# Kernel optimization log

Hardware: AMD Instinct MI355X
Metric: run time of the kernel (lower is better)

## Reference

```python
import jax, jax.numpy as jnp
import numpy as np

B, N, M, DN, DE, WN, WE, P = 16, 128, 1024, 512, 256, 128, 128, 512
EMB = WN + WE            # nenn embedding size per node / per edge
CLS_IN = 2 * EMB // 1    # = 2*wn + 2*we = 512
LR_OUT, CR_OUT, MR_OUT = 9, 6, 17
HID = 256


def _mk_params(key):
    ks = jax.random.split(key, 16)
    s = 0.02
    p = {
        'Wn':  jax.random.normal(ks[0], (DN, WN), jnp.float32) * s,
        'We':  jax.random.normal(ks[1], (DE, WE), jnp.float32) * s,
        'Wn2': jax.random.normal(ks[2], (DN, WN), jnp.float32) * s,
        'We2': jax.random.normal(ks[3], (DE, WE), jnp.float32) * s,
    }
    for i, h in enumerate(['scr', 'lr', 'mr']):
        out = {'scr': CR_OUT, 'lr': LR_OUT, 'mr': MR_OUT}[h]
        p[h + '_W1'] = jax.random.normal(ks[4 + 4 * i], (2 * EMB, HID), jnp.float32) * s
        p[h + '_b1'] = jnp.zeros((HID,), jnp.float32)
        p[h + '_W2'] = jax.random.normal(ks[5 + 4 * i], (HID, out), jnp.float32) * s
        p[h + '_b2'] = jnp.zeros((out,), jnp.float32)
    return p


def setup_inputs() -> dict:
    key = jax.random.key(0)
    ks = jax.random.split(key, 10)
    inp = {
        'node_features': jax.random.normal(ks[0], (B, N, DN), jnp.float32),
        'edge_features': jax.random.normal(ks[1], (B, N, N, DE), jnp.float32),
        'adj_mat': (jax.random.uniform(ks[2], (B, N, N)) < 0.1).astype(jnp.float32),
        'line_adj_mat': (jax.random.uniform(ks[3], (B, M, M)) < 0.02).astype(jnp.float32),
        'edge_index': jax.random.randint(ks[4], (B, 2, M), 0, N, jnp.int32),
        'object_pairs': jax.random.randint(ks[5], (B, P, 2), 0, N, jnp.int32),
        'num_obj': jax.random.randint(ks[6], (B,), N // 4, N + 1, jnp.int32),
        'num_edges': jax.random.randint(ks[7], (B,), M // 4, M + 1, jnp.int32),
    }
    inp.update(_mk_params(ks[8]))
    return inp


def _mlp(x, W1, b1, W2, b2):
    return jax.nn.relu(x @ W1 + b1) @ W2 + b2


def _forward(node_features, edge_features, adj_mat, line_adj_mat,
             Wn, We, Wn2, We2,
             scr_W1, scr_b1, scr_W2, scr_b2,
             lr_W1, lr_b1, lr_W2, lr_b2,
             mr_W1, mr_b1, mr_W2, mr_b2,
             edge_index, object_pairs, num_obj, num_edges):
    dt = node_features.dtype
    # ragged slicing [:num_obj] / [:num_edges] expressed as masks (padding stays 0)
    nmask = (jnp.arange(N) < num_obj[:, None]).astype(dt)      # [B,N]
    emask = (jnp.arange(M) < num_edges[:, None]).astype(dt)    # [B,M]

    X = node_features * nmask[..., None]                        # [B,N,DN]
    A = (adj_mat * nmask[:, :, None] * nmask[:, None, :]
         + jnp.eye(N, dtype=dt)[None] * nmask[:, :, None])      # A + I, masked
    h = jax.nn.relu((A @ X) @ Wn) * nmask[..., None]            # [B,N,WN] node-level emb

    src, dst = edge_index[:, 0], edge_index[:, 1]               # [B,M]
    Eg = jax.vmap(lambda e, s, d: e[s, d])(edge_features, src, dst)  # [B,M,DE]
    Eg = Eg * emask[..., None]
    L = (line_adj_mat * emask[:, :, None] * emask[:, None, :]
         + jnp.eye(M, dtype=dt)[None] * emask[:, :, None])      # line graph A + I
    g = jax.nn.relu((L @ Eg) @ We) * emask[..., None]           # [B,M,WE] edge-level emb

    # aggregate edge embeddings onto their source nodes (ragged scatter-add)
    agg = jax.vmap(lambda gb, sb: jnp.zeros((N, WE), gb.dtype).at[sb].add(gb))(g, src)
    node_emb = jnp.concatenate([h, agg * nmask[..., None]], -1)  # [B,N,EMB]

    # dense pairwise edge embeddings [B,N,N,EMB]
    Xp = X @ Wn2                                                 # [B,N,WN]
    Pm = jax.nn.relu(Xp[:, :, None, :] + Xp[:, None, :, :])      # node part [B,N,N,WN]
    Q = jax.nn.relu(edge_features @ We2)                         # edge part [B,N,N,WE]
    edge_emb = jnp.concatenate([Pm, Q], -1)

    # make_classifier_inputs: fused ragged gather instead of python double loop
    p0, p1 = object_pairs[..., 0], object_pairs[..., 1]          # [B,P]
    emb0 = jnp.take_along_axis(node_emb, p0[:, :, None], axis=1)  # [B,P,EMB]
    emb1 = jnp.take_along_axis(node_emb, p1[:, :, None], axis=1)
    eedge = jax.vmap(lambda eb, a, b: eb[a, b])(edge_emb, p0, p1)  # [B,P,EMB]
    ci = jnp.concatenate([emb0 + emb1, eedge], -1)               # aggregator='sum'

    lr = _mlp(ci, lr_W1, lr_b1, lr_W2, lr_b2)
    cr = _mlp(ci, scr_W1, scr_b1, scr_W2, scr_b2)
    mr = _mlp(ci, mr_W1, mr_b1, mr_W2, mr_b2)
    return lr, cr, mr


def reference(node_features, edge_features, adj_mat, line_adj_mat,
              edge_index, object_pairs, num_obj, num_edges,
              Wn, We, Wn2, We2,
              scr_W1, scr_b1, scr_W2, scr_b2,
              lr_W1, lr_b1, lr_W2, lr_b2,
              mr_W1, mr_b1, mr_W2, mr_b2):
    return _forward(node_features, edge_features, adj_mat, line_adj_mat,
                    Wn, We, Wn2, We2,
                    scr_W1, scr_b1, scr_W2, scr_b2,
                    lr_W1, lr_b1, lr_W2, lr_b2,
                    mr_W1, mr_b1, mr_W2, mr_b2,
                    edge_index, object_pairs, num_obj, num_edges)
```

## Files before the change

kernel.cpp:

```cpp
#include <hip/hip_runtime.h>
#include <hip/hip_bf16.h>
#include <cstdint>
#include <cstddef>

#define BB 16
#define NN 128
#define MM 1024
#define DN 512
#define DE 256
#define WN 128
#define WE 128
#define PP 512
#define HIDW 256
#define CIW 512

typedef __attribute__((ext_vector_type(8))) short s16x8;
typedef __attribute__((ext_vector_type(4))) float f32x4;

__device__ __forceinline__ float bf2f(unsigned short u) {
    unsigned int x = ((unsigned int)u) << 16;
    union { unsigned int i; float f; } c; c.i = x; return c.f;
}
__device__ __forceinline__ short f2b(float f) {
    __hip_bfloat16 h = __float2bfloat16(f);
    return *reinterpret_cast<short*>(&h);
}

__device__ __forceinline__ void gl_lds16(const ushort* g, ushort* l) {
    __builtin_amdgcn_global_load_lds(
        (const __attribute__((address_space(1))) unsigned int*)g,
        (__attribute__((address_space(3))) unsigned int*)l,
        16, 0, 0);
}

__global__ __launch_bounds__(256) void k0_prep(
    const float* __restrict__ lrW1, const float* __restrict__ scrW1,
    const float* __restrict__ mrW1,
    const float* __restrict__ lrb1, const float* __restrict__ scrb1,
    const float* __restrict__ mrb1,
    const float* __restrict__ Wn, const float* __restrict__ Wn2,
    const float* __restrict__ We, const float* __restrict__ We2,
    __hip_bfloat16* __restrict__ W1t, __hip_bfloat16* __restrict__ WncT,
    __hip_bfloat16* __restrict__ WeT, __hip_bfloat16* __restrict__ We2T,
    float* __restrict__ b1cat)
{
    int blk = blockIdx.x;
    int t = threadIdx.x;
    if (blk < 768) {
        int h = blk >> 8, n = blk & 255;
        const float* W = (h == 0) ? lrW1 : (h == 1) ? scrW1 : mrW1;
        W1t[(size_t)blk * 512 + t]       = __float2bfloat16(W[t * 256 + n]);
        W1t[(size_t)blk * 512 + t + 256] = __float2bfloat16(W[(t + 256) * 256 + n]);
    } else if (blk == 768) {
        b1cat[t]       = lrb1[t];
        b1cat[256 + t] = scrb1[t];
        b1cat[512 + t] = mrb1[t];
    } else if (blk < 897) {
        int n = blk - 769;
        WeT[(size_t)n * 256 + t] = __float2bfloat16(We[t * 128 + n]);
    } else if (blk < 1153) {
        int n = blk - 897;
        const float* W = (n < 128) ? Wn : Wn2;
        int c = n & 127;
        WncT[(size_t)n * 512 + t]       = __float2bfloat16(W[t * 128 + c]);
        WncT[(size_t)n * 512 + t + 256] = __float2bfloat16(W[(t + 256) * 128 + c]);
    } else {
        int n = blk - 1153;
        We2T[(size_t)n * 256 + t] = __float2bfloat16(We2[t * 128 + n]);
    }
}

__global__ __launch_bounds__(256) void fproj(
    const float* __restrict__ nf, const float* __restrict__ ef,
    const int* __restrict__ eidx, const int* __restrict__ opair,
    const int* __restrict__ nobj, const int* __restrict__ nedg,
    const ushort* __restrict__ WncT, const ushort* __restrict__ WeT,
    const ushort* __restrict__ We2T,
    float* __restrict__ Y, float* __restrict__ Xp,
    float* __restrict__ G1, __hip_bfloat16* __restrict__ ci)
{
    __shared__ ushort As[128 * 32];
    __shared__ ushort Bs[128 * 32];
    __shared__ unsigned rowoff[128];
    __shared__ float    rowval[128];

    int blk = blockIdx.x;
    int route, mb, nb, K;
    const ushort* Bt;
    if (blk < 32)       { route = 0; mb = blk >> 1;  nb = blk & 1; K = 512; Bt = WncT; }
    else if (blk < 160) { route = 1; mb = blk - 32;  nb = 0;       K = 256; Bt = WeT;  }
    else                { route = 2; mb = blk - 160; nb = 0;       K = 256; Bt = We2T; }
    int row0 = mb * 128, col0 = nb * 128;
    int t = threadIdx.x;

    if (t < 128) {
        int r = row0 + t;
        unsigned off; float valid = 1.f;
        if (route == 0) {
            int b = r >> 7, i = r & 127;
            off = (unsigned)r * DN;
            valid = (i < nobj[b]) ? 1.f : 0.f;
        } else if (route == 1) {
            int b = r >> 10, m = r & 1023;
            int src = eidx[b * 2 * MM + m];
            int dst = eidx[b * 2 * MM + MM + m];
            off = (unsigned)((b * NN + src) * NN + dst) * DE;
            valid = (m < nedg[b]) ? 1.f : 0.f;
        } else {
            int r2 = r;
            int b = r2 >> 9, p = r2 & 511;
            int i0 = opair[(b * PP + p) * 2];
            int i1 = opair[(b * PP + p) * 2 + 1];
            off = (unsigned)((b * NN + i0) * NN + i1) * DE;
        }
        rowoff[t] = off; rowval[t] = valid;
    }

    const float* Asrc = (route == 0) ? nf : ef;
    int lane = t & 63;
    int w    = t >> 6;
    int wr   = w >> 1, wc = w & 1;
    int arow = w * 32 + (lane >> 2);
    int ak   = (lane & 3) * 8;
    int qk   = (lane >> 4) * 8;
    int fr   = lane & 15;
    int sr   = t >> 2;
    int sk   = (t & 3) * 8;
    f32x4 acc[4][4];
    #pragma unroll
    for (int i = 0; i < 4; ++i)
        #pragma unroll
        for (int j = 0; j < 4; ++j) acc[i][j] = (f32x4){0.f, 0.f, 0.f, 0.f};

    for (int k0 = 0; k0 < K; k0 += 32) {
        __syncthreads();
        gl_lds16(&Bt[(size_t)(col0 + sr) * K + k0 + sk],      &Bs[t * 8]);
        gl_lds16(&Bt[(size_t)(col0 + sr + 64) * K + k0 + sk], &Bs[t * 8 + 2048]);
        {
            unsigned o0 = rowoff[arow] + k0 + ak;
            unsigned o1 = rowoff[arow + 16] + k0 + ak;
            float m0 = rowval[arow], m1 = rowval[arow + 16];
            float4 a0 = *(const float4*)&Asrc[o0];
            float4 a1 = *(const float4*)&Asrc[o0 + 4];
            float4 b0 = *(const float4*)&Asrc[o1];
            float4 b1 = *(const float4*)&Asrc[o1 + 4];
            s16x8 pa, pb;
            pa[0]=f2b(a0.x*m0); pa[1]=f2b(a0.y*m0); pa[2]=f2b(a0.z*m0); pa[3]=f2b(a0.w*m0);
            pa[4]=f2b(a1.x*m0); pa[5]=f2b(a1.y*m0); pa[6]=f2b(a1.z*m0); pa[7]=f2b(a1.w*m0);
            pb[0]=f2b(b0.x*m1); pb[1]=f2b(b0.y*m1); pb[2]=f2b(b0.z*m1); pb[3]=f2b(b0.w*m1);
            pb[4]=f2b(b1.x*m1); pb[5]=f2b(b1.y*m1); pb[6]=f2b(b1.z*m1); pb[7]=f2b(b1.w*m1);
            *(s16x8*)&As[arow * 32 + ak]        = pa;
            *(s16x8*)&As[(arow + 16) * 32 + ak] = pb;
        }
        __syncthreads();
        s16x8 af[4], bfv[4];
        #pragma unroll
        for (int mi = 0; mi < 4; ++mi)
            af[mi] = *(const s16x8*)&As[(wr * 64 + mi * 16 + fr) * 32 + qk];
        #pragma unroll
        for (int ni = 0; ni < 4; ++ni)
            bfv[ni] = *(const s16x8*)&Bs[(wc * 64 + ni * 16 + fr) * 32 + qk];
        #pragma unroll
        for (int mi = 0; mi < 4; ++mi)
            #pragma unroll
            for (int ni = 0; ni < 4; ++ni)
                acc[mi][ni] = __builtin_amdgcn_mfma_f32_16x16x32_bf16(
                    af[mi], bfv[ni], acc[mi][ni], 0, 0, 0);
    }
    int crow = (lane >> 4) * 4;
    #pragma unroll
    for (int mi = 0; mi < 4; ++mi) {
        #pragma unroll
        for (int ni = 0; ni < 4; ++ni) {
            int gc = col0 + wc * 64 + ni * 16 + fr;
            int gr = row0 + wr * 64 + mi * 16 + crow;
            #pragma unroll
            for (int rg = 0; rg < 4; ++rg) {
                float v = acc[mi][ni][rg];
                int r = gr + rg;
                if (route == 0) {
                    if (gc < 128) Y [(size_t)r * WN + gc]       = v;
                    else          Xp[(size_t)r * WN + gc - 128] = v;
                } else if (route == 1) {
                    G1[(size_t)r * WE + gc] = v;
                } else {
                    ci[(size_t)r * CIW + 384 + gc] = __float2bfloat16(fmaxf(v, 0.f));
                }
            }
        }
    }
}

__global__ __launch_bounds__(256) void k2_gcn_node(
    const float* __restrict__ adj, const int* __restrict__ num_obj,
    const float* __restrict__ Y, float* __restrict__ node_emb)
{
    __shared__ float As[16 * 129];
    int b  = blockIdx.x >> 4;
    int i0 = ((blockIdx.x >> 1) & 7) * 16;
    int ch = blockIdx.x & 1;
    int s  = num_obj[b];
    int t  = threadIdx.x;
    if (t < 128) {
        for (int rr = 0; rr < 16; ++rr) {
            int i = i0 + rr;
            float v = 0.f;
            if (i < s) {
                v = adj[(size_t)(b * NN + i) * NN + t] * ((t < s) ? 1.f : 0.f);
                if (t == i) v += 1.f;
            }
            As[rr * 129 + t] = v;
        }
    }
    __syncthreads();
    int c  = ch * 64 + (t & 63);
    int rb = (t >> 6) * 4;
    float acc[4] = {0.f,0.f,0.f,0.f};
    for (int j = 0; j < NN; ++j) {
        float yv = Y[(b * NN + j) * WN + c];
        #pragma unroll
        for (int r = 0; r < 4; ++r) acc[r] += As[(rb + r) * 129 + j] * yv;
    }
    #pragma unroll
    for (int r = 0; r < 4; ++r) {
        int i = i0 + rb + r;
        node_emb[(b * NN + i) * 256 + c]       = fmaxf(acc[r], 0.f);
        node_emb[(b * NN + i) * 256 + 128 + c] = 0.f;
    }
}

__global__ __launch_bounds__(128) void k4_line_gcn(
    const float* __restrict__ la, const float* __restrict__ G1,
    const int* __restrict__ eidx, const int* __restrict__ num_edges,
    float* __restrict__ node_emb)
{
    int b = blockIdx.x >> 10;
    int m = blockIdx.x & 1023;
    int se = num_edges[b];
    if (m >= se) return;
    __shared__ int   cnt;
    __shared__ int   idxs[MM];
    __shared__ float vals[MM];
    int t = threadIdx.x;
    if (t == 0) cnt = 0;
    __syncthreads();
    const float* larow = la + ((size_t)b * MM + m) * MM;
    for (int it = 0; it < 8; ++it) {
        int j = it * 128 + t;
        float v = larow[j];
        if (v != 0.f) {
            int pos = atomicAdd(&cnt, 1);
            idxs[pos] = j;
            vals[pos] = v;
        }
    }
    __syncthreads();
    int n = cnt;
    const float* g1b = G1 + (size_t)b * MM * WE;
    float acc = g1b[m * WE + t];
    for (int p = 0; p < n; ++p)
        acc += vals[p] * g1b[idxs[p] * WE + t];
    float g = fmaxf(acc, 0.f);
    int src = eidx[b * 2 * MM + m];
    atomicAdd(&node_emb[(b * NN + src) * 256 + 128 + t], g);
}

__global__ __launch_bounds__(256) void k5a_build_ci(
    const float* __restrict__ node_emb, const float* __restrict__ Xp,
    const int* __restrict__ opairs, const int* __restrict__ num_obj,
    __hip_bfloat16* __restrict__ ci)
{
    __shared__ int   pi0[16], pi1[16];
    __shared__ float nm0[16], nm1[16];
    int b     = blockIdx.x >> 5;
    int pbase = (blockIdx.x & 31) * 16;
    int t     = threadIdx.x;
    int s     = num_obj[b];
    if (t < 16) {
        int p  = pbase + t;
        int i0 = opairs[(b * PP + p) * 2];
        int i1 = opairs[(b * PP + p) * 2 + 1];
        pi0[t] = i0; pi1[t] = i1;
        nm0[t] = (i0 < s) ? 1.f : 0.f;
        nm1[t] = (i1 < s) ? 1.f : 0.f;
    }
    __syncthreads();
    for (int pp = 0; pp < 16; ++pp) {
        int i0 = pi0[pp], i1 = pi1[pp];
        int p  = pbase + pp;
        __hip_bfloat16* cirow = ci + (size_t)(b * PP + p) * CIW;
        float m0f = (t < 128) ? 1.f : nm0[pp];
        float m1f = (t < 128) ? 1.f : nm1[pp];
        float v = node_emb[(b * NN + i0) * 256 + t] * m0f
                + node_emb[(b * NN + i1) * 256 + t] * m1f;
        cirow[t] = __float2bfloat16(v);
        if (t < 128) {
            float pm = Xp[(b * NN + i0) * WN + t] + Xp[(b * NN + i1) * WN + t];
            cirow[256 + t] = __float2bfloat16(fmaxf(pm, 0.f));
        }
    }
}

__global__ __launch_bounds__(256) void k6_mlp1_mfma(
    const ushort* __restrict__ A,
    const ushort* __restrict__ Bt,
    const float* __restrict__ b1cat,
    __hip_bfloat16* __restrict__ H)
{
    __shared__ ushort As[128 * 32];
    __shared__ ushort Bs[128 * 32];
    int t    = threadIdx.x;
    int col0 = blockIdx.x * 128;
    int row0 = blockIdx.y * 128;
    int lane = t & 63;
    int w    = t >> 6;
    int wr   = w >> 1, wc = w & 1;
    int qk   = (lane >> 4) * 8;
    int fr   = lane & 15;
    int sr   = t >> 2;
    int sk   = (t & 3) * 8;
    f32x4 acc[4][4];
    #pragma unroll
    for (int i = 0; i < 4; ++i)
        #pragma unroll
        for (int j = 0; j < 4; ++j) acc[i][j] = (f32x4){0.f, 0.f, 0.f, 0.f};

    for (int k0 = 0; k0 < CIW; k0 += 32) {
        __syncthreads();
        gl_lds16(&A [(size_t)(row0 + sr) * CIW + k0 + sk],      &As[t * 8]);
        gl_lds16(&A [(size_t)(row0 + sr + 64) * CIW + k0 + sk], &As[t * 8 + 2048]);
        gl_lds16(&Bt[(size_t)(col0 + sr) * CIW + k0 + sk],      &Bs[t * 8]);
        gl_lds16(&Bt[(size_t)(col0 + sr + 64) * CIW + k0 + sk], &Bs[t * 8 + 2048]);
        __syncthreads();
        s16x8 af[4], bfv[4];
        #pragma unroll
        for (int mi = 0; mi < 4; ++mi)
            af[mi] = *(const s16x8*)&As[(wr * 64 + mi * 16 + fr) * 32 + qk];
        #pragma unroll
        for (int ni = 0; ni < 4; ++ni)
            bfv[ni] = *(const s16x8*)&Bs[(wc * 64 + ni * 16 + fr) * 32 + qk];
        #pragma unroll
        for (int mi = 0; mi < 4; ++mi)
            #pragma unroll
            for (int ni = 0; ni < 4; ++ni)
                acc[mi][ni] = __builtin_amdgcn_mfma_f32_16x16x32_bf16(
                    af[mi], bfv[ni], acc[mi][ni], 0, 0, 0);
    }
    int crow = (lane >> 4) * 4;
    #pragma unroll
    for (int mi = 0; mi < 4; ++mi) {
        #pragma unroll
        for (int ni = 0; ni < 4; ++ni) {
            int gc = col0 + wc * 64 + ni * 16 + fr;
            int gr = row0 + wr * 64 + mi * 16 + crow;
            float bias = b1cat[gc];
            #pragma unroll
            for (int rg = 0; rg < 4; ++rg) {
                float v = fmaxf(acc[mi][ni][rg] + bias, 0.f);
                H[(size_t)(gr + rg) * 768 + gc] = __float2bfloat16(v);
            }
        }
    }
}

__global__ __launch_bounds__(256) void k7_mlp2(
    const __hip_bfloat16* __restrict__ H,
    const float* __restrict__ lrW2, const float* __restrict__ lrb2,
    const float* __restrict__ scrW2, const float* __restrict__ scrb2,
    const float* __restrict__ mrW2, const float* __restrict__ mrb2,
    float* __restrict__ outp)
{
    __shared__ float w2s[32 * 257];
    int t = threadIdx.x;
    for (int o = 0; o < 32; ++o) {
        float v;
        if (o < 9)       v = lrW2[t * 9 + o];
        else if (o < 15) v = scrW2[t * 6 + (o - 9)];
        else             v = mrW2[t * 17 + (o - 15)];
        w2s[o * 257 + t] = v;
    }
    __syncthreads();
    int p = blockIdx.x * 8 + (t >> 5);
    int o = t & 31;
    int seg = (o < 9) ? 0 : ((o < 15) ? 1 : 2);
    const ushort* hr = (const ushort*)H + (size_t)p * 768 + seg * 256;
    const float* wr = &w2s[o * 257];
    float acc = (o < 9) ? lrb2[o] : ((o < 15) ? scrb2[o - 9] : mrb2[o - 15]);
    for (int k = 0; k < HIDW; k += 8) {
        s16x8 u = *(const s16x8*)&hr[k];
        acc += bf2f((unsigned short)u[0]) * wr[k]
             + bf2f((unsigned short)u[1]) * wr[k + 1]
             + bf2f((unsigned short)u[2]) * wr[k + 2]
             + bf2f((unsigned short)u[3]) * wr[k + 3]
             + bf2f((unsigned short)u[4]) * wr[k + 4]
             + bf2f((unsigned short)u[5]) * wr[k + 5]
             + bf2f((unsigned short)u[6]) * wr[k + 6]
             + bf2f((unsigned short)u[7]) * wr[k + 7];
    }
    if (o < 9)       outp[(size_t)p * 9 + o] = acc;
    else if (o < 15) outp[8192 * 9 + (size_t)p * 6 + (o - 9)] = acc;
    else             outp[8192 * 15 + (size_t)p * 17 + (o - 15)] = acc;
}

extern "C" void kernel_launch(void* const* d_in, const int* in_sizes, int n_in,
                              void* d_out, int out_size, void* d_ws, size_t ws_size,
                              hipStream_t stream) {
    const float* nf    = (const float*)d_in[0];
    const float* ef    = (const float*)d_in[1];
    const float* adj   = (const float*)d_in[2];
    const float* la    = (const float*)d_in[3];
    const int*   eidx  = (const int*)d_in[4];
    const int*   opair = (const int*)d_in[5];
    const int*   nobj  = (const int*)d_in[6];
    const int*   nedg  = (const int*)d_in[7];
    const float* Wn    = (const float*)d_in[8];
    const float* We    = (const float*)d_in[9];
    const float* Wn2   = (const float*)d_in[10];
    const float* We2   = (const float*)d_in[11];
    const float* scrW1 = (const float*)d_in[12];
    const float* scrb1 = (const float*)d_in[13];
    const float* scrW2 = (const float*)d_in[14];
    const float* scrb2 = (const float*)d_in[15];
    const float* lrW1  = (const float*)d_in[16];
    const float* lrb1  = (const float*)d_in[17];
    const float* lrW2  = (const float*)d_in[18];
    const float* lrb2  = (const float*)d_in[19];
    const float* mrW1  = (const float*)d_in[20];
    const float* mrb1  = (const float*)d_in[21];
    const float* mrW2  = (const float*)d_in[22];
    const float* mrb2  = (const float*)d_in[23];

    float* ws = (float*)d_ws;
    float* Y        = ws;
    float* Xp       = Y + 262144;
    float* node_emb = Xp + 262144;
    float* G1       = node_emb + 524288;
    float* base     = G1 + 2097152;
    __hip_bfloat16* ci   = (__hip_bfloat16*)base;
    __hip_bfloat16* hid  = (__hip_bfloat16*)(base + 2097152);
    __hip_bfloat16* W1t  = (__hip_bfloat16*)(base + 2097152 + 3145728);
    __hip_bfloat16* WncT = (__hip_bfloat16*)(base + 2097152 + 3145728 + 196608);
    __hip_bfloat16* WeT  = (__hip_bfloat16*)(base + 2097152 + 3145728 + 196608 + 65536);
    __hip_bfloat16* We2T = (__hip_bfloat16*)(base + 2097152 + 3145728 + 196608 + 65536 + 16384);
    float* b1cat = base + 2097152 + 3145728 + 196608 + 65536 + 16384 + 16384;

    k0_prep <<<1281, 256, 0, stream>>>(lrW1, scrW1, mrW1, lrb1, scrb1, mrb1,
                                       Wn, Wn2, We, We2,
                                       W1t, WncT, WeT, We2T, b1cat);
    fproj   <<<224, 256, 0, stream>>>(nf, ef, eidx, opair, nobj, nedg,
                                      (const ushort*)WncT, (const ushort*)WeT,
                                      (const ushort*)We2T, Y, Xp, G1, ci);
    k2_gcn_node <<<BB * 8 * 2, 256, 0, stream>>>(adj, nobj, Y, node_emb);
    k4_line_gcn <<<BB * MM, 128, 0, stream>>>(la, G1, eidx, nedg, node_emb);
    k5a_build_ci<<<BB * (PP / 16), 256, 0, stream>>>(node_emb, Xp, opair, nobj, ci);
    k6_mlp1_mfma<<<dim3(6, 64), 256, 0, stream>>>((const ushort*)ci,
                                                  (const ushort*)W1t, b1cat, hid);
    k7_mlp2     <<<8192 / 8, 256, 0, stream>>>(hid, lrW2, lrb2, scrW2, scrb2,
                                               mrW2, mrb2, (float*)d_out);
}
```

Baseline: 473.1 us.

## Drop weight-prep kernel, convert weights inline, merge node and line GCN kernels

Removes the separate weight transpose/convert kernel. The fproj and MLP1 GEMMs now read fp32 weights directly, convert them to bf16 and store them into a swizzled LDS layout. The node GCN and line-graph GCN kernels are fused into one launch, and the line GCN handles two edges per 256-thread block with float4 scans of the adjacency row. The zeroing of the aggregation buffer moves into extra fproj blocks. This cuts launches and intermediate weight buffers, but adds strided scalar global weight loads inside the GEMM k-loops.

```diff
diff --git a/kernel.cpp b/kernel.cpp
--- a/kernel.cpp
+++ b/kernel.cpp
@@ -25,7 +25,6 @@
     __hip_bfloat16 h = __float2bfloat16(f);
     return *reinterpret_cast<short*>(&h);
 }
-
 __device__ __forceinline__ void gl_lds16(const ushort* g, ushort* l) {
     __builtin_amdgcn_global_load_lds(
         (const __attribute__((address_space(1))) unsigned int*)g,
@@ -33,65 +32,40 @@
         16, 0, 0);
 }
 
-__global__ __launch_bounds__(256) void k0_prep(
-    const float* __restrict__ lrW1, const float* __restrict__ scrW1,
-    const float* __restrict__ mrW1,
-    const float* __restrict__ lrb1, const float* __restrict__ scrb1,
-    const float* __restrict__ mrb1,
-    const float* __restrict__ Wn, const float* __restrict__ Wn2,
-    const float* __restrict__ We, const float* __restrict__ We2,
-    __hip_bfloat16* __restrict__ W1t, __hip_bfloat16* __restrict__ WncT,
-    __hip_bfloat16* __restrict__ WeT, __hip_bfloat16* __restrict__ We2T,
-    float* __restrict__ b1cat)
-{
-    int blk = blockIdx.x;
-    int t = threadIdx.x;
-    if (blk < 768) {
-        int h = blk >> 8, n = blk & 255;
-        const float* W = (h == 0) ? lrW1 : (h == 1) ? scrW1 : mrW1;
-        W1t[(size_t)blk * 512 + t]       = __float2bfloat16(W[t * 256 + n]);
-        W1t[(size_t)blk * 512 + t + 256] = __float2bfloat16(W[(t + 256) * 256 + n]);
-    } else if (blk == 768) {
-        b1cat[t]       = lrb1[t];
-        b1cat[256 + t] = scrb1[t];
-        b1cat[512 + t] = mrb1[t];
-    } else if (blk < 897) {
-        int n = blk - 769;
-        WeT[(size_t)n * 256 + t] = __float2bfloat16(We[t * 128 + n]);
-    } else if (blk < 1153) {
-        int n = blk - 897;
-        const float* W = (n < 128) ? Wn : Wn2;
-        int c = n & 127;
-        WncT[(size_t)n * 512 + t]       = __float2bfloat16(W[t * 128 + c]);
-        WncT[(size_t)n * 512 + t + 256] = __float2bfloat16(W[(t + 256) * 128 + c]);
-    } else {
-        int n = blk - 1153;
-        We2T[(size_t)n * 256 + t] = __float2bfloat16(We2[t * 128 + n]);
-    }
-}
+#define BSWZ(row, q) ((q) ^ (((row) & 3) << 3))
 
 __global__ __launch_bounds__(256) void fproj(
     const float* __restrict__ nf, const float* __restrict__ ef,
     const int* __restrict__ eidx, const int* __restrict__ opair,
     const int* __restrict__ nobj, const int* __restrict__ nedg,
-    const ushort* __restrict__ WncT, const ushort* __restrict__ WeT,
-    const ushort* __restrict__ We2T,
+    const float* __restrict__ Wn, const float* __restrict__ Wn2,
+    const float* __restrict__ We, const float* __restrict__ We2,
     float* __restrict__ Y, float* __restrict__ Xp,
-    float* __restrict__ G1, __hip_bfloat16* __restrict__ ci)
+    float* __restrict__ G1, __hip_bfloat16* __restrict__ ci,
+    float* __restrict__ AGG)
 {
+    int blk = blockIdx.x;
+    int t   = threadIdx.x;
+
+    if (blk >= 224) {
+        float4* a4 = (float4*)AGG;
+        int base = (blk - 224) * 256 + t;
+        #pragma unroll
+        for (int i = 0; i < 8; ++i) a4[base + i * 8192] = (float4){0.f,0.f,0.f,0.f};
+        return;
+    }
+
     __shared__ ushort As[128 * 32];
     __shared__ ushort Bs[128 * 32];
     __shared__ unsigned rowoff[128];
     __shared__ float    rowval[128];
 
-    int blk = blockIdx.x;
-    int route, mb, nb, K;
-    const ushort* Bt;
-    if (blk < 32)       { route = 0; mb = blk >> 1;  nb = blk & 1; K = 512; Bt = WncT; }
-    else if (blk < 160) { route = 1; mb = blk - 32;  nb = 0;       K = 256; Bt = WeT;  }
-    else                { route = 2; mb = blk - 160; nb = 0;       K = 256; Bt = We2T; }
-    int row0 = mb * 128, col0 = nb * 128;
-    int t = threadIdx.x;
+    int route, mb, nbk, K;
+    const float* Wsrc;
+    if (blk < 32)       { route = 0; mb = blk >> 1;  nbk = blk & 1; K = 512; Wsrc = nbk ? Wn2 : Wn; }
+    else if (blk < 160) { route = 1; mb = blk - 32;  nbk = 0;       K = 256; Wsrc = We;  }
+    else                { route = 2; mb = blk - 160; nbk = 0;       K = 256; Wsrc = We2; }
+    int row0 = mb * 128, col0 = nbk * 128;
 
     if (t < 128) {
         int r = row0 + t;
@@ -107,8 +81,7 @@
             off = (unsigned)((b * NN + src) * NN + dst) * DE;
             valid = (m < nedg[b]) ? 1.f : 0.f;
         } else {
-            int r2 = r;
-            int b = r2 >> 9, p = r2 & 511;
+            int b = r >> 9, p = r & 511;
             int i0 = opair[(b * PP + p) * 2];
             int i1 = opair[(b * PP + p) * 2 + 1];
             off = (unsigned)((b * NN + i0) * NN + i1) * DE;
@@ -124,8 +97,8 @@
     int ak   = (lane & 3) * 8;
     int qk   = (lane >> 4) * 8;
     int fr   = lane & 15;
-    int sr   = t >> 2;
-    int sk   = (t & 3) * 8;
+    int nid  = t & 127;
+    int koct = t >> 7;
     f32x4 acc[4][4];
     #pragma unroll
     for (int i = 0; i < 4; ++i)
@@ -134,8 +107,15 @@
 
     for (int k0 = 0; k0 < K; k0 += 32) {
         __syncthreads();
-        gl_lds16(&Bt[(size_t)(col0 + sr) * K + k0 + sk],      &Bs[t * 8]);
-        gl_lds16(&Bt[(size_t)(col0 + sr + 64) * K + k0 + sk], &Bs[t * 8 + 2048]);
+        #pragma unroll
+        for (int p = 0; p < 2; ++p) {
+            int kk0 = (koct + 2 * p) * 8;
+            s16x8 pw;
+            #pragma unroll
+            for (int i = 0; i < 8; ++i)
+                pw[i] = f2b(Wsrc[(size_t)(k0 + kk0 + i) * 128 + nid]);
+            *(s16x8*)&Bs[nid * 32 + BSWZ(nid, kk0)] = pw;
+        }
         {
             unsigned o0 = rowoff[arow] + k0 + ak;
             unsigned o1 = rowoff[arow + 16] + k0 + ak;
@@ -158,8 +138,10 @@
         for (int mi = 0; mi < 4; ++mi)
             af[mi] = *(const s16x8*)&As[(wr * 64 + mi * 16 + fr) * 32 + qk];
         #pragma unroll
-        for (int ni = 0; ni < 4; ++ni)
-            bfv[ni] = *(const s16x8*)&Bs[(wc * 64 + ni * 16 + fr) * 32 + qk];
+        for (int ni = 0; ni < 4; ++ni) {
+            int rr = wc * 64 + ni * 16 + fr;
+            bfv[ni] = *(const s16x8*)&Bs[rr * 32 + BSWZ(rr, qk)];
+        }
         #pragma unroll
         for (int mi = 0; mi < 4; ++mi)
             #pragma unroll
@@ -191,83 +173,95 @@
     }
 }
 
-__global__ __launch_bounds__(256) void k2_gcn_node(
-    const float* __restrict__ adj, const int* __restrict__ num_obj,
-    const float* __restrict__ Y, float* __restrict__ node_emb)
+__global__ __launch_bounds__(256) void k24(
+    const float* __restrict__ adj, const int* __restrict__ nobj,
+    const float* __restrict__ Y, float* __restrict__ neh,
+    const float* __restrict__ la, const float* __restrict__ G1,
+    const int* __restrict__ eidx, const int* __restrict__ nedg,
+    float* __restrict__ AGG)
 {
-    __shared__ float As[16 * 129];
-    int b  = blockIdx.x >> 4;
-    int i0 = ((blockIdx.x >> 1) & 7) * 16;
-    int ch = blockIdx.x & 1;
-    int s  = num_obj[b];
-    int t  = threadIdx.x;
-    if (t < 128) {
-        for (int rr = 0; rr < 16; ++rr) {
-            int i = i0 + rr;
-            float v = 0.f;
-            if (i < s) {
-                v = adj[(size_t)(b * NN + i) * NN + t] * ((t < s) ? 1.f : 0.f);
-                if (t == i) v += 1.f;
+    __shared__ union {
+        struct { float As[16 * 129]; } k2;
+        struct { int idxs[2][MM]; float vals[2][MM]; int cnt[2]; } k4;
+    } S;
+    int t = threadIdx.x;
+
+    if (blockIdx.x < 256) {
+        int vb = blockIdx.x;
+        int b  = vb >> 4;
+        int i0 = ((vb >> 1) & 7) * 16;
+        int ch = vb & 1;
+        int s  = nobj[b];
+        if (t < 128) {
+            for (int rr = 0; rr < 16; ++rr) {
+                int i = i0 + rr;
+                float v = 0.f;
+                if (i < s) {
+                    v = adj[(size_t)(b * NN + i) * NN + t] * ((t < s) ? 1.f : 0.f);
+                    if (t == i) v += 1.f;
+                }
+                S.k2.As[rr * 129 + t] = v;
             }
-            As[rr * 129 + t] = v;
-        }
-    }
-    __syncthreads();
-    int c  = ch * 64 + (t & 63);
-    int rb = (t >> 6) * 4;
-    float acc[4] = {0.f,0.f,0.f,0.f};
-    for (int j = 0; j < NN; ++j) {
-        float yv = Y[(b * NN + j) * WN + c];
-        #pragma unroll
-        for (int r = 0; r < 4; ++r) acc[r] += As[(rb + r) * 129 + j] * yv;
-    }
-    #pragma unroll
-    for (int r = 0; r < 4; ++r) {
-        int i = i0 + rb + r;
-        node_emb[(b * NN + i) * 256 + c]       = fmaxf(acc[r], 0.f);
-        node_emb[(b * NN + i) * 256 + 128 + c] = 0.f;
-    }
-}
-
-__global__ __launch_bounds__(128) void k4_line_gcn(
-    const float* __restrict__ la, const float* __restrict__ G1,
-    const int* __restrict__ eidx, const int* __restrict__ num_edges,
-    float* __restrict__ node_emb)
-{
-    int b = blockIdx.x >> 10;
-    int m = blockIdx.x & 1023;
-    int se = num_edges[b];
-    if (m >= se) return;
-    __shared__ int   cnt;
-    __shared__ int   idxs[MM];
-    __shared__ float vals[MM];
-    int t = threadIdx.x;
-    if (t == 0) cnt = 0;
-    __syncthreads();
-    const float* larow = la + ((size_t)b * MM + m) * MM;
-    for (int it = 0; it < 8; ++it) {
-        int j = it * 128 + t;
-        float v = larow[j];
-        if (v != 0.f) {
-            int pos = atomicAdd(&cnt, 1);
-            idxs[pos] = j;
-            vals[pos] = v;
-        }
-    }
-    __syncthreads();
-    int n = cnt;
-    const float* g1b = G1 + (size_t)b * MM * WE;
-    float acc = g1b[m * WE + t];
-    for (int p = 0; p < n; ++p)
-        acc += vals[p] * g1b[idxs[p] * WE + t];
-    float g = fmaxf(acc, 0.f);
-    int src = eidx[b * 2 * MM + m];
-    atomicAdd(&node_emb[(b * NN + src) * 256 + 128 + t], g);
+        }
+        __syncthreads();
+        int c  = ch * 64 + (t & 63);
+        int rb = (t >> 6) * 4;
+        float acc[4] = {0.f, 0.f, 0.f, 0.f};
+        for (int j = 0; j < NN; ++j) {
+            float yv = Y[(b * NN + j) * WN + c];
+            #pragma unroll
+            for (int r = 0; r < 4; ++r) acc[r] += S.k2.As[(rb + r) * 129 + j] * yv;
+        }
+        #pragma unroll
+        for (int r = 0; r < 4; ++r) {
+            int i = i0 + rb + r;
+            neh[(b * NN + i) * 128 + c] = fmaxf(acc[r], 0.f);
+        }
+    } else {
+        int vb = blockIdx.x - 256;
+        int half = t >> 7;
+        int ch   = t & 127;
+        int b = vb >> 9;
+        int m = (vb & 511) * 2 + half;
+        int se = nedg[b];
+        bool act = (m < se);
+        if (ch == 0) S.k4.cnt[half] = 0;
+        __syncthreads();
+        if (act) {
+            const float4* larow = (const float4*)(la + ((size_t)b * MM + m) * MM);
+            #pragma unroll
+            for (int pass = 0; pass < 2; ++pass) {
+                int j4 = pass * 128 + ch;
+                float4 v = larow[j4];
+                int j0 = j4 * 4;
+                int nl = (v.x != 0.f) + (v.y != 0.f) + (v.z != 0.f) + (v.w != 0.f);
+                if (nl) {
+                    int p = atomicAdd(&S.k4.cnt[half], nl);
+                    if (v.x != 0.f) { S.k4.idxs[half][p] = j0;     S.k4.vals[half][p] = v.x; ++p; }
+                    if (v.y != 0.f) { S.k4.idxs[half][p] = j0 + 1; S.k4.vals[half][p] = v.y; ++p; }
+                    if (v.z != 0.f) { S.k4.idxs[half][p] = j0 + 2; S.k4.vals[half][p] = v.z; ++p; }
+                    if (v.w != 0.f) { S.k4.idxs[half][p] = j0 + 3; S.k4.vals[half][p] = v.w; }
+                }
+            }
+        }
+        __syncthreads();
+        if (act) {
+            int n = S.k4.cnt[half];
+            const float* g1b = G1 + (size_t)b * MM * WE;
+            float acc = g1b[m * WE + ch];
+            for (int p = 0; p < n; ++p)
+                acc += S.k4.vals[half][p] * g1b[S.k4.idxs[half][p] * WE + ch];
+            float gv = fmaxf(acc, 0.f);
+            int src = eidx[b * 2 * MM + m];
+            atomicAdd(&AGG[((size_t)b * NN + src) * 128 + ch], gv);
+        }
+    }
 }
 
 __global__ __launch_bounds__(256) void k5a_build_ci(
-    const float* __restrict__ node_emb, const float* __restrict__ Xp,
-    const int* __restrict__ opairs, const int* __restrict__ num_obj,
+    const float* __restrict__ neh, const float* __restrict__ AGG,
+    const float* __restrict__ Xp,
+    const int* __restrict__ opairs, const int* __restrict__ nobj,
     __hip_bfloat16* __restrict__ ci)
 {
     __shared__ int   pi0[16], pi1[16];
@@ -275,7 +269,7 @@
     int b     = blockIdx.x >> 5;
     int pbase = (blockIdx.x & 31) * 16;
     int t     = threadIdx.x;
-    int s     = num_obj[b];
+    int s     = nobj[b];
     if (t < 16) {
         int p  = pbase + t;
         int i0 = opairs[(b * PP + p) * 2];
@@ -289,10 +283,14 @@
         int i0 = pi0[pp], i1 = pi1[pp];
         int p  = pbase + pp;
         __hip_bfloat16* cirow = ci + (size_t)(b * PP + p) * CIW;
-        float m0f = (t < 128) ? 1.f : nm0[pp];
-        float m1f = (t < 128) ? 1.f : nm1[pp];
-        float v = node_emb[(b * NN + i0) * 256 + t] * m0f
-                + node_emb[(b * NN + i1) * 256 + t] * m1f;
+        float v;
+        if (t < 128) {
+            v = neh[(b * NN + i0) * 128 + t] + neh[(b * NN + i1) * 128 + t];
+        } else {
+            int c = t - 128;
+            v = AGG[(b * NN + i0) * 128 + c] * nm0[pp]
+              + AGG[(b * NN + i1) * 128 + c] * nm1[pp];
+        }
         cirow[t] = __float2bfloat16(v);
         if (t < 128) {
             float pm = Xp[(b * NN + i0) * WN + t] + Xp[(b * NN + i1) * WN + t];
@@ -303,8 +301,10 @@
 
 __global__ __launch_bounds__(256) void k6_mlp1_mfma(
     const ushort* __restrict__ A,
-    const ushort* __restrict__ Bt,
-    const float* __restrict__ b1cat,
+    const float* __restrict__ lrW1, const float* __restrict__ scrW1,
+    const float* __restrict__ mrW1,
+    const float* __restrict__ lrb1, const float* __restrict__ scrb1,
+    const float* __restrict__ mrb1,
     __hip_bfloat16* __restrict__ H)
 {
     __shared__ ushort As[128 * 32];
@@ -312,6 +312,9 @@
     int t    = threadIdx.x;
     int col0 = blockIdx.x * 128;
     int row0 = blockIdx.y * 128;
+    const float* W1h = (col0 < 256) ? lrW1 : (col0 < 512) ? scrW1 : mrW1;
+    const float* bh  = (col0 < 256) ? lrb1 : (col0 < 512) ? scrb1 : mrb1;
+    int cih = col0 & 255;
     int lane = t & 63;
     int w    = t >> 6;
     int wr   = w >> 1, wc = w & 1;
@@ -319,6 +322,8 @@
     int fr   = lane & 15;
     int sr   = t >> 2;
     int sk   = (t & 3) * 8;
+    int nid  = t & 127;
+    int koct = t >> 7;
     f32x4 acc[4][4];
     #pragma unroll
     for (int i = 0; i < 4; ++i)
@@ -327,18 +332,27 @@
 
     for (int k0 = 0; k0 < CIW; k0 += 32) {
         __syncthreads();
-        gl_lds16(&A [(size_t)(row0 + sr) * CIW + k0 + sk],      &As[t * 8]);
-        gl_lds16(&A [(size_t)(row0 + sr + 64) * CIW + k0 + sk], &As[t * 8 + 2048]);
-        gl_lds16(&Bt[(size_t)(col0 + sr) * CIW + k0 + sk],      &Bs[t * 8]);
-        gl_lds16(&Bt[(size_t)(col0 + sr + 64) * CIW + k0 + sk], &Bs[t * 8 + 2048]);
+        gl_lds16(&A[(size_t)(row0 + sr) * CIW + k0 + sk],      &As[t * 8]);
+        gl_lds16(&A[(size_t)(row0 + sr + 64) * CIW + k0 + sk], &As[t * 8 + 2048]);
+        #pragma unroll
+        for (int p = 0; p < 2; ++p) {
+            int kk0 = (koct + 2 * p) * 8;
+            s16x8 pw;
+            #pragma unroll
+            for (int i = 0; i < 8; ++i)
+                pw[i] = f2b(W1h[(size_t)(k0 + kk0 + i) * 256 + cih + nid]);
+            *(s16x8*)&Bs[nid * 32 + BSWZ(nid, kk0)] = pw;
+        }
         __syncthreads();
         s16x8 af[4], bfv[4];
         #pragma unroll
         for (int mi = 0; mi < 4; ++mi)
             af[mi] = *(const s16x8*)&As[(wr * 64 + mi * 16 + fr) * 32 + qk];
         #pragma unroll
-        for (int ni = 0; ni < 4; ++ni)
-            bfv[ni] = *(const s16x8*)&Bs[(wc * 64 + ni * 16 + fr) * 32 + qk];
+        for (int ni = 0; ni < 4; ++ni) {
+            int rr = wc * 64 + ni * 16 + fr;
+            bfv[ni] = *(const s16x8*)&Bs[rr * 32 + BSWZ(rr, qk)];
+        }
         #pragma unroll
         for (int mi = 0; mi < 4; ++mi)
             #pragma unroll
@@ -353,7 +367,7 @@
         for (int ni = 0; ni < 4; ++ni) {
             int gc = col0 + wc * 64 + ni * 16 + fr;
             int gr = row0 + wr * 64 + mi * 16 + crow;
-            float bias = b1cat[gc];
+            float bias = bh[gc & 255];
             #pragma unroll
             for (int rg = 0; rg < 4; ++rg) {
                 float v = fmaxf(acc[mi][ni][rg] + bias, 0.f);
@@ -431,30 +445,22 @@
     const float* mrb2  = (const float*)d_in[23];
 
     float* ws = (float*)d_ws;
-    float* Y        = ws;
-    float* Xp       = Y + 262144;
-    float* node_emb = Xp + 262144;
-    float* G1       = node_emb + 524288;
-    float* base     = G1 + 2097152;
-    __hip_bfloat16* ci   = (__hip_bfloat16*)base;
-    __hip_bfloat16* hid  = (__hip_bfloat16*)(base + 2097152);
-    __hip_bfloat16* W1t  = (__hip_bfloat16*)(base + 2097152 + 3145728);
-    __hip_bfloat16* WncT = (__hip_bfloat16*)(base + 2097152 + 3145728 + 196608);
-    __hip_bfloat16* WeT  = (__hip_bfloat16*)(base + 2097152 + 3145728 + 196608 + 65536);
-    __hip_bfloat16* We2T = (__hip_bfloat16*)(base + 2097152 + 3145728 + 196608 + 65536 + 16384);
-    float* b1cat = base + 2097152 + 3145728 + 196608 + 65536 + 16384 + 16384;
-
-    k0_prep <<<1281, 256, 0, stream>>>(lrW1, scrW1, mrW1, lrb1, scrb1, mrb1,
-                                       Wn, Wn2, We, We2,
-                                       W1t, WncT, WeT, We2T, b1cat);
-    fproj   <<<224, 256, 0, stream>>>(nf, ef, eidx, opair, nobj, nedg,
-                                      (const ushort*)WncT, (const ushort*)WeT,
-                                      (const ushort*)We2T, Y, Xp, G1, ci);
-    k2_gcn_node <<<BB * 8 * 2, 256, 0, stream>>>(adj, nobj, Y, node_emb);
-    k4_line_gcn <<<BB * MM, 128, 0, stream>>>(la, G1, eidx, nedg, node_emb);
-    k5a_build_ci<<<BB * (PP / 16), 256, 0, stream>>>(node_emb, Xp, opair, nobj, ci);
+    float* Y    = ws;
+    float* Xp   = Y + 262144;
+    float* neh  = Xp + 262144;
+    float* AGG  = neh + 262144;
+    float* G1   = AGG + 262144;
+    float* base = G1 + 2097152;
+    __hip_bfloat16* ci  = (__hip_bfloat16*)base;
+    __hip_bfloat16* hid = (__hip_bfloat16*)(base + 2097152);
+
+    fproj<<<256, 256, 0, stream>>>(nf, ef, eidx, opair, nobj, nedg,
+                                   Wn, Wn2, We, We2, Y, Xp, G1, ci, AGG);
+    k24  <<<8448, 256, 0, stream>>>(adj, nobj, Y, neh, la, G1, eidx, nedg, AGG);
+    k5a_build_ci<<<BB * (PP / 16), 256, 0, stream>>>(neh, AGG, Xp, opair, nobj, ci);
     k6_mlp1_mfma<<<dim3(6, 64), 256, 0, stream>>>((const ushort*)ci,
-                                                  (const ushort*)W1t, b1cat, hid);
+                                                  lrW1, scrW1, mrW1,
+                                                  lrb1, scrb1, mrb1, hid);
     k7_mlp2     <<<8192 / 8, 256, 0, stream>>>(hid, lrW2, lrb2, scrW2, scrb2,
                                                mrW2, mrb2, (float*)d_out);
 }
```

Result: faster. 459.4 us (-2.9%).
